# Optimization experiments

Measured on AMD Instinct MI355X. Metric: run time of the kernel, lower is better.

Reference implementation:

```python
import jax, jax.numpy as jnp
import numpy as np

SIZE = 128
WIN = SIZE // 4   # sliding-window size == region size (32)
HALF = WIN // 2   # 16


def _conv(x, w, pad, groups=1):
    return jax.lax.conv_general_dilated(x, w, (1, 1), [(pad, pad), (pad, pad)],
        dimension_numbers=('NCHW', 'OIHW', 'NCHW'), feature_group_count=groups)


def _resize(x, h, w):
    # F.interpolate(..., mode='bilinear', align_corners=False)
    return jax.image.resize(x, (x.shape[0], x.shape[1], h, w), 'bilinear', antialias=False)


def _gauss_kernels():
    ax = np.linspace(-2.0, 2.0, 5)
    xx, yy = np.meshgrid(ax, ax)
    g = np.exp(-(xx ** 2 + yy ** 2) / 2.0) / (2.0 * np.pi)  # sigma = 1
    gx = (-xx * g).astype(np.float32)
    gy = (-yy * g).astype(np.float32)
    return (jnp.asarray(np.tile(gx[None, None], (3, 3, 1, 1))),
            jnp.asarray(np.tile(gy[None, None], (3, 3, 1, 1))))


def _edge_extract(x):
    Gx, Gy = _gauss_kernels()
    h = _conv(x, Gx, 2)
    v = _conv(x, Gy, 2)
    return jnp.tanh(jnp.sqrt(h * h + v * v + 1e-8))


def _color_moments(x, win=5):
    # F.unfold-based local mean / unbiased var / skewness, via depthwise box sums
    C = x.shape[1]
    n = float(win * win)
    ones = jnp.ones((C, 1, win, win), x.dtype)
    box = lambda z: _conv(z, ones, win // 2, groups=C)
    s1 = box(x); s2 = box(x * x); s3 = box(x * x * x)
    mean = s1 / n
    var = (s2 - n * mean * mean) / (n - 1.0)               # unbiased, matches torch.var
    m3 = (s3 - 3.0 * mean * s2 + 2.0 * n * mean ** 3) / n  # E[(x-m)^3]
    skew = m3 / (jnp.sqrt(jnp.maximum(var, 0.0)) ** 3 + 1e-6)
    return jnp.concatenate([mean, var, skew], 1)


def _locate_region(c):
    # scipy: gradient magnitude < 0.2 -> 4-connected label at argmax -> bbox center
    H, W = c.shape
    flat = jnp.argmax(c)
    xm = (flat // W).astype(jnp.int32)
    ym = (flat % W).astype(jnp.int32)
    gm = jnp.hypot(jnp.gradient(c, axis=0), jnp.gradient(c, axis=1))
    mask = gm < 0.2
    seed = jnp.zeros((H, W), bool).at[xm, ym].set(True) & mask

    def dil(r):
        d = r
        d = d | jnp.pad(r[1:, :], ((0, 1), (0, 0)))
        d = d | jnp.pad(r[:-1, :], ((1, 0), (0, 0)))
        d = d | jnp.pad(r[:, 1:], ((0, 0), (0, 1)))
        d = d | jnp.pad(r[:, :-1], ((0, 0), (1, 0)))
        return d & mask

    def body(s):
        r, _ = s
        nr = dil(r)
        return (nr, jnp.any(nr != r))

    region, _ = jax.lax.while_loop(lambda s: s[1], body, (seed, jnp.any(seed)))
    rows = jnp.any(region, 1); cols = jnp.any(region, 0)
    rs = jnp.argmax(rows); re = H - jnp.argmax(rows[::-1])
    cs = jnp.argmax(cols); ce = W - jnp.argmax(cols[::-1])
    ok = mask[xm, ym]  # label_at_max != 0
    x1 = jnp.where(ok, ((rs + re) // 2).astype(jnp.int32), xm)
    y1 = jnp.where(ok, ((cs + ce) // 2).astype(jnp.int32), ym)
    return x1, y1


def _affine_grid(move, H, W):
    # theta = [[1,0,tx],[0,1,ty]] with (tx,ty)=move, align_corners=False
    bx = (2.0 * jnp.arange(W, dtype=jnp.float32) + 1.0) / W - 1.0
    by = (2.0 * jnp.arange(H, dtype=jnp.float32) + 1.0) / H - 1.0
    gx = bx[None, None, :] + move[:, 0, None, None]
    gy = by[None, :, None] + move[:, 1, None, None]
    return jnp.stack(jnp.broadcast_arrays(gx, gy), -1)  # [B,H,W,2]


def _grid_sample(x, grid):
    # bilinear, zeros padding, align_corners=False (torch defaults)
    B, C, H, W = x.shape
    ix = ((grid[..., 0] + 1.0) * W - 1.0) / 2.0
    iy = ((grid[..., 1] + 1.0) * H - 1.0) / 2.0
    ix0 = jnp.floor(ix).astype(jnp.int32)
    iy0 = jnp.floor(iy).astype(jnp.int32)
    wx1 = ix - ix0; wy1 = iy - iy0
    b = jnp.arange(B)[:, None, None]

    def g(yy, xx):
        valid = ((xx >= 0) & (xx < W) & (yy >= 0) & (yy < H)).astype(x.dtype)
        v = x[b, :, jnp.clip(yy, 0, H - 1), jnp.clip(xx, 0, W - 1)]  # [B,Hg,Wg,C]
        return v * valid[..., None]

    out = (g(iy0, ix0) * ((1 - wy1) * (1 - wx1))[..., None]
         + g(iy0, ix0 + 1) * ((1 - wy1) * wx1)[..., None]
         + g(iy0 + 1, ix0) * (wy1 * (1 - wx1))[..., None]
         + g(iy0 + 1, ix0 + 1) * (wy1 * wx1)[..., None])
    return jnp.transpose(out, (0, 3, 1, 2))


def _bn_relu6(x, w, b):
    # BatchNorm2d in training mode (batch stats, biased var, eps=1e-5) + ReLU6
    m = x.mean((0, 2, 3), keepdims=True)
    v = ((x - m) ** 2).mean((0, 2, 3), keepdims=True)
    y = (x - m) / jnp.sqrt(v + 1e-5) * w[None, :, None, None] + b[None, :, None, None]
    return jnp.clip(y, 0.0, 6.0)


def setup_inputs():
    key = jax.random.key(0)
    ks = jax.random.split(key, 8)
    B, C = 8, 64
    return dict(
        warm_flag=1,
        feat1=jax.random.normal(ks[0], (B, C, SIZE, SIZE), jnp.float32),
        feat2=jax.random.normal(ks[1], (B, C, SIZE, SIZE), jnp.float32),
        cam1=jax.random.uniform(ks[2], (B, 64, 64), jnp.float32),
        cam2=jax.random.uniform(ks[3], (B, 64, 64), jnp.float32),
        f_g=jax.random.uniform(ks[4], (B, 3, 512, 512), jnp.float32),
        f_e=jax.random.uniform(ks[5], (B, 3, 512, 512), jnp.float32),
        conv1_w=jax.random.normal(ks[6], (C, 3, 3, 3), jnp.float32) * 0.1,
        conv1_b=jnp.zeros((C,), jnp.float32),
        conv2_w=jax.random.normal(ks[7], (C, 9, 3, 3), jnp.float32) * 0.1,
        conv2_b=jnp.zeros((C,), jnp.float32),
        bn_w=jnp.ones((C,), jnp.float32),
        bn_b=jnp.zeros((C,), jnp.float32),
    )


def reference(warm_flag, feat1, feat2, cam1, cam2, f_g, f_e,
              conv1_w, conv1_b, conv2_w, conv2_b, bn_w, bn_b):
    B = cam1.shape[0]
    c1 = _resize(cam1[:, None], SIZE, SIZE)
    c2 = _resize(cam2[:, None], SIZE, SIZE)

    if warm_flag == 1:
        # numpy/scipy path in torch is detached from autograd
        c1s = jax.lax.stop_gradient(c1)
        c2s = jax.lax.stop_gradient(c2)
        x1, y1 = jax.vmap(_locate_region)(c1s[:, 0])
        # valid-mode box convolution of cam2 with ones((H//4, W//4)), argmax
        box = jax.lax.conv_general_dilated(c2s, jnp.ones((1, 1, WIN, WIN), c2.dtype), (1, 1),
            'VALID', dimension_numbers=('NCHW', 'OIHW', 'NCHW'))[:, 0]
        Wv = box.shape[-1]
        flat = jnp.argmax(box.reshape(B, -1), -1)
        x2 = (flat // Wv + HALF).astype(jnp.int32)
        y2 = (flat % Wv + HALF).astype(jnp.int32)

        idx = jnp.arange(SIZE)
        def rect(xc, yc):
            r = (idx[None, :] >= jnp.maximum(xc - HALF, 0)[:, None]) & \
                (idx[None, :] < jnp.minimum(xc + HALF, SIZE)[:, None])
            cc = (idx[None, :] >= jnp.maximum(yc - HALF, 0)[:, None]) & \
                 (idx[None, :] < jnp.minimum(yc + HALF, SIZE)[:, None])
            return r[:, None, :, None] & cc[:, None, None, :]
        mask1 = rect(x1, y1).astype(feat1.dtype)
        mask2 = rect(x2, y2).astype(feat2.dtype)
        mi1 = jnp.stack([x1, y1], -1).astype(jnp.float32)
        mi2 = jnp.stack([x2, y2], -1).astype(jnp.float32)
    else:
        mask1 = jnp.zeros_like(feat1)
        mask2 = jnp.zeros_like(feat2)
        mi1 = jnp.zeros((B, 2), jnp.float32)
        mi2 = jnp.zeros((B, 2), jnp.float32)

    cam2_move = (mi2 - mi1) / (SIZE // 2)
    cam1_move = (mi1 - mi2) / (SIZE // 2)
    grid1 = _affine_grid(cam1_move, SIZE, SIZE)
    grid2 = _affine_grid(cam2_move, SIZE, SIZE)

    moments = _resize(_color_moments(f_e), SIZE, SIZE)   # [B,9,128,128]
    edge = _resize(_edge_extract(f_g), SIZE, SIZE)       # [B,3,128,128]
    feat1_edge = jnp.clip(_conv(edge, conv1_w, 1) + conv1_b[None, :, None, None], 0.0, 6.0)
    feat2_color = _conv(moments, conv2_w, 1) + conv2_b[None, :, None, None]

    feat2_move = _grid_sample(feat2_color * mask2, grid2)
    feat1_edge_move = _grid_sample(feat1_edge * mask1, grid1)

    Bc, C, H, W = feat1.shape
    f1 = feat1.reshape(Bc, C, -1)
    f2 = feat2.reshape(Bc, C, -1)
    f2m = feat2_move.reshape(Bc, C, -1)
    f1m = feat1_edge_move.reshape(Bc, C, -1)

    f2_attn = jax.nn.softmax(jnp.einsum('bcn,bdn->bcd', f2m, f1), -1)  # [B,C,C]
    feat1_apply = jnp.einsum('bcd,bdn->bcn', f2_attn, f1).reshape(Bc, C, H, W)
    f1_attn = jax.nn.softmax(jnp.einsum('bcn,bdn->bcd', f1m, f2), -1)
    feat2_apply = jnp.einsum('bcd,bdn->bcn', f1_attn, f2).reshape(Bc, C, H, W)

    feat1_apply = _bn_relu6(feat1_apply, bn_w, bn_b)
    feat2_apply = _bn_relu6(feat2_apply, bn_w, bn_b)

    if warm_flag == 0:
        return (feat1, feat2, grid1, grid2, feat1_edge, feat2_color, f1_attn, f2_attn, feat1, feat2)
    return (feat1_apply, feat2_apply, grid1, grid2, feat1_edge, feat2_color, f1_attn, f2_attn, feat1, feat2)
```

## Files before the change

kernel.cpp:

```cpp
#include <hip/hip_runtime.h>
#include <math.h>

#define SIZE 128
#define WIN 32
#define HALF 16
#define B 8
#define C 64
#define N (SIZE*SIZE)
#define BCN 8388608
#define BV 97

#define O_APPLY1   0
#define O_APPLY2   8388608
#define O_GRID1    16777216
#define O_GRID2    17039360
#define O_EDGEF    17301504
#define O_COLORF   25690112
#define O_ATTN1    34078720
#define O_ATTN2    34111488
#define O_FEAT1    34144256
#define O_FEAT2    42532864

#define WS_C1      0
#define WS_C2      131072
#define WS_COLSUM  262144
#define WS_XY      361472
#define WS_MOM     361600
#define WS_EDGE    1541248
#define WS_LOG1    1672320
#define WS_LOG2    1705088
#define WS_BN      1737856

#define NEGINF (-3.402823466e+38f)

typedef unsigned __int128 u128;

__global__ void k_init(float* __restrict__ p, int n) {
  int i = blockIdx.x * 256 + threadIdx.x;
  if (i < n) p[i] = 0.f;
}

__global__ __launch_bounds__(256) void k_resize_cam(
    const float* __restrict__ cam1, const float* __restrict__ cam2,
    float* __restrict__ c1, float* __restrict__ c2) {
  int idx = blockIdx.x * 256 + threadIdx.x;
  int which = idx >> 17;
  int rem = idx & 131071;
  int b = rem >> 14, i = (rem >> 7) & 127, j = rem & 127;
  const float* s = (which ? cam2 : cam1) + b * 4096;
  float fy = fminf(fmaxf(0.5f * (float)i - 0.25f, 0.f), 63.f);
  float fx = fminf(fmaxf(0.5f * (float)j - 0.25f, 0.f), 63.f);
  int y0 = (int)fy; float ty = fy - (float)y0; int y1i = min(y0 + 1, 63);
  int x0 = (int)fx; float tx = fx - (float)x0; int x1i = min(x0 + 1, 63);
  float v00 = s[y0 * 64 + x0],  v01 = s[y0 * 64 + x1i];
  float v10 = s[y1i * 64 + x0], v11 = s[y1i * 64 + x1i];
  float v = (1.f - ty) * ((1.f - tx) * v00 + tx * v01)
          + ty * ((1.f - tx) * v10 + tx * v11);
  (which ? c2 : c1)[rem] = v;
}

__device__ __forceinline__ u128 hfill(u128 g, u128 m) {
  u128 p = m;
  g |= p & (g << 1);  p &= p << 1;
  g |= p & (g << 2);  p &= p << 2;
  g |= p & (g << 4);  p &= p << 4;
  g |= p & (g << 8);  p &= p << 8;
  g |= p & (g << 16); p &= p << 16;
  g |= p & (g << 32); p &= p << 32;
  g |= p & (g << 64);
  p = m;
  g |= p & (g >> 1);  p &= p >> 1;
  g |= p & (g >> 2);  p &= p >> 2;
  g |= p & (g >> 4);  p &= p >> 4;
  g |= p & (g >> 8);  p &= p >> 8;
  g |= p & (g >> 16); p &= p >> 16;
  g |= p & (g >> 32); p &= p >> 32;
  g |= p & (g >> 64);
  return g;
}

__global__ __launch_bounds__(256) void k_locate(const float* __restrict__ c1,
                                                int* __restrict__ xy) {
  int b = blockIdx.x;
  const float* c = c1 + b * N;
  int tid = threadIdx.x;
  __shared__ float sc[N];
  __shared__ float sv[256]; __shared__ int si[256];
  __shared__ unsigned int maskw[512];
  __shared__ unsigned long long glo[128], ghi[128];
  __shared__ unsigned long long rowany[2];
  __shared__ int s_changed, s_xm, s_ym, s_ok;

  float bv = NEGINF; int bi = 0;
  const float4* c4 = (const float4*)c;
  float4* sc4 = (float4*)sc;
  #pragma unroll
  for (int k = 0; k < 16; ++k) {
    int i4 = k * 256 + tid;
    float4 v = c4[i4];
    sc4[i4] = v;
    int base = i4 * 4;
    if (v.x > bv) { bv = v.x; bi = base; }
    if (v.y > bv) { bv = v.y; bi = base + 1; }
    if (v.z > bv) { bv = v.z; bi = base + 2; }
    if (v.w > bv) { bv = v.w; bi = base + 3; }
  }
  sv[tid] = bv; si[tid] = bi;
  __syncthreads();
  for (int s = 128; s; s >>= 1) {
    if (tid < s) {
      float ov = sv[tid + s]; int oi = si[tid + s];
      if (ov > sv[tid] || (ov == sv[tid] && oi < si[tid])) { sv[tid] = ov; si[tid] = oi; }
    }
    __syncthreads();
  }
  if (tid == 0) { s_xm = si[0] >> 7; s_ym = si[0] & 127; }

  #pragma unroll
  for (int q = 0; q < 2; ++q) {
    int w = tid + q * 256;
    int row = w >> 2, cb = (w & 3) * 32;
    unsigned int m = 0;
    for (int bit = 0; bit < 32; ++bit) {
      int i = row, j = cb + bit;
      float gx_, gy_;
      if (i == 0)        gx_ = sc[128 + j] - sc[j];
      else if (i == 127) gx_ = sc[127 * 128 + j] - sc[126 * 128 + j];
      else               gx_ = 0.5f * (sc[(i + 1) * 128 + j] - sc[(i - 1) * 128 + j]);
      if (j == 0)        gy_ = sc[i * 128 + 1] - sc[i * 128];
      else if (j == 127) gy_ = sc[i * 128 + 127] - sc[i * 128 + 126];
      else               gy_ = 0.5f * (sc[i * 128 + j + 1] - sc[i * 128 + j - 1]);
      if (hypotf(gx_, gy_) < 0.2f) m |= (1u << bit);
    }
    maskw[w] = m;
  }
  __syncthreads();
  if (tid == 0) {
    int w = (s_xm << 2) + (s_ym >> 5), bit = s_ym & 31;
    s_ok = (maskw[w] >> bit) & 1;
  }
  __syncthreads();

  int r = tid;
  u128 m = 0, g = 0;
  if (tid < 128) {
    m = ((u128)maskw[r * 4])
      | ((u128)maskw[r * 4 + 1] << 32)
      | ((u128)maskw[r * 4 + 2] << 64)
      | ((u128)maskw[r * 4 + 3] << 96);
    if (s_ok && r == s_xm) g = ((u128)1) << s_ym;
    g = hfill(g, m);
  }
  for (;;) {
    if (tid == 0) s_changed = 0;
    if (tid < 128) { glo[r] = (unsigned long long)g; ghi[r] = (unsigned long long)(g >> 64); }
    __syncthreads();
    if (tid < 128) {
      u128 gn = g;
      if (r > 0)   gn |= ((u128)glo[r - 1]) | ((u128)ghi[r - 1] << 64);
      if (r < 127) gn |= ((u128)glo[r + 1]) | ((u128)ghi[r + 1] << 64);
      gn &= m;
      gn = hfill(gn, m);
      if (gn != g) { g = gn; s_changed = 1; }
    }
    __syncthreads();
    if (!s_changed) break;
  }

  if (tid < 128) {
    unsigned long long ba = __ballot(g != 0);
    if ((tid & 63) == 0) rowany[tid >> 6] = ba;
    glo[r] = (unsigned long long)g; ghi[r] = (unsigned long long)(g >> 64);
  }
  __syncthreads();
  if (tid == 0) {
    unsigned long long r0 = rowany[0], r1 = rowany[1];
    unsigned long long cl = 0, ch = 0;
    for (int i = 0; i < 128; ++i) { cl |= glo[i]; ch |= ghi[i]; }
    int rs = 0, re = 0, cs = 0, ce = 0;
    if (r0 | r1) {
      rs = r0 ? (__ffsll(r0) - 1) : 64 + (__ffsll(r1) - 1);
      re = r1 ? 128 - __clzll(r1) : 64 - __clzll(r0);
      cs = cl ? (__ffsll(cl) - 1) : 64 + (__ffsll(ch) - 1);
      ce = ch ? 128 - __clzll(ch) : 64 - __clzll(cl);
    }
    int x1, y1;
    if (s_ok) { x1 = (rs + re) >> 1; y1 = (cs + ce) >> 1; }
    else      { x1 = s_xm;           y1 = s_ym; }
    xy[b] = x1; xy[8 + b] = y1;
  }
}

__global__ __launch_bounds__(256) void k_colsum(const float* __restrict__ c2,
                                                float* __restrict__ cs) {
  int idx = blockIdx.x * 256 + threadIdx.x;
  if (idx >= B * BV * 128) return;
  int cc = idx & 127, r = (idx >> 7) % BV, b = idx / (BV * 128);
  const float* s = c2 + b * N + cc;
  float acc = 0.f;
  #pragma unroll
  for (int dy = 0; dy < WIN; ++dy) acc += s[(r + dy) * 128];
  cs[idx] = acc;
}

__global__ __launch_bounds__(256) void k_boxargmax(const float* __restrict__ colsum,
                                                   int* __restrict__ xy) {
  int b = blockIdx.x, tid = threadIdx.x;
  const float* cs = colsum + b * BV * 128;
  float bv = NEGINF; int bi = 0;
  for (int p = tid; p < BV * BV; p += 256) {
    int r = p / BV, cc = p % BV;
    const float* row = cs + r * 128 + cc;
    float s = 0.f;
    #pragma unroll
    for (int dx = 0; dx < WIN; ++dx) s += row[dx];
    if (s > bv) { bv = s; bi = p; }
  }
  __shared__ float sv[256]; __shared__ int si[256];
  sv[tid] = bv; si[tid] = bi;
  __syncthreads();
  for (int s = 128; s; s >>= 1) {
    if (tid < s) {
      float ov = sv[tid + s]; int oi = si[tid + s];
      if (ov > sv[tid] || (ov == sv[tid] && oi < si[tid])) { sv[tid] = ov; si[tid] = oi; }
    }
    __syncthreads();
  }
  if (tid == 0) { xy[16 + b] = si[0] / BV + HALF; xy[24 + b] = si[0] % BV + HALF; }
}

__global__ __launch_bounds__(256) void k_grids(const int* __restrict__ xy,
                                               float* __restrict__ g1, float* __restrict__ g2) {
  int idx = blockIdx.x * 256 + threadIdx.x;
  int b = idx >> 14, h = (idx >> 7) & 127, w = idx & 127;
  float x1 = (float)xy[b], y1 = (float)xy[8 + b];
  float x2 = (float)xy[16 + b], y2 = (float)xy[24 + b];
  float bx = (2.f * (float)w + 1.f) / 128.f - 1.f;
  float by = (2.f * (float)h + 1.f) / 128.f - 1.f;
  float m1x = (x1 - x2) / 64.f, m1y = (y1 - y2) / 64.f;
  g1[idx * 2]     = bx + m1x; g1[idx * 2 + 1] = by + m1y;
  g2[idx * 2]     = bx - m1x; g2[idx * 2 + 1] = by - m1y;
}

__global__ __launch_bounds__(256) void k_moments(const float* __restrict__ fe,
                                                 float* __restrict__ mom) {
  int idx = blockIdx.x * 256 + threadIdx.x;
  int j = idx & 127, i = (idx >> 7) & 127, ch = (idx >> 14) % 3, b = idx / (3 * N);
  const float* src = fe + (size_t)(b * 3 + ch) * 262144;
  float s1a[6], s2a[6], s3a[6], s1b[6], s2b[6], s3b[6];
  #pragma unroll
  for (int t = 0; t < 6; ++t) {
    float a1 = 0, a2 = 0, a3 = 0, b1 = 0, b2 = 0, b3 = 0;
    int x = 4 * j - 1 + t;
    bool xo = (x >= 0 && x < 512);
    #pragma unroll
    for (int r = 0; r < 6; ++r) {
      int y = 4 * i - 1 + r;
      float v = (xo && y >= 0 && y < 512) ? src[y * 512 + x] : 0.f;
      float v2 = v * v, v3 = v2 * v;
      if (r < 5) { a1 += v; a2 += v2; a3 += v3; }
      if (r > 0) { b1 += v; b2 += v2; b3 += v3; }
    }
    s1a[t] = a1; s2a[t] = a2; s3a[t] = a3;
    s1b[t] = b1; s2b[t] = b2; s3b[t] = b3;
  }
  float am = 0, av = 0, as = 0;
  #pragma unroll
  for (int py = 0; py < 2; ++py) {
    #pragma unroll
    for (int px = 0; px < 2; ++px) {
      float s1 = 0, s2 = 0, s3 = 0;
      #pragma unroll
      for (int t = 0; t < 5; ++t) {
        s1 += py ? s1b[px + t] : s1a[px + t];
        s2 += py ? s2b[px + t] : s2a[px + t];
        s3 += py ? s3b[px + t] : s3a[px + t];
      }
      float mean = s1 / 25.f;
      float var  = (s2 - 25.f * mean * mean) / 24.f;
      float m3   = (s3 - 3.f * mean * s2 + 50.f * mean * mean * mean) / 25.f;
      float sq   = sqrtf(fmaxf(var, 0.f));
      float skew = m3 / (sq * sq * sq + 1e-6f);
      am += mean; av += var; as += skew;
    }
  }
  int base = (b * 9 + ch) * N + i * 128 + j;
  mom[base]         = 0.25f * am;
  mom[base + 3 * N] = 0.25f * av;
  mom[base + 6 * N] = 0.25f * as;
}

__global__ __launch_bounds__(256) void k_edge(const float* __restrict__ fg,
                                              float* __restrict__ edge) {
  int idx = blockIdx.x * 256 + threadIdx.x;
  int j = idx & 127, i = (idx >> 7) & 127, b = idx >> 14;
  const float* s0 = fg + (size_t)b * 3 * 262144;
  const float INV2PI = 0.15915494309189535f;
  float wg[5], ug[5];
  #pragma unroll
  for (int t = 0; t < 5; ++t) {
    float a = (float)t - 2.f;
    float e = expf(-0.5f * a * a);
    wg[t] = e; ug[t] = -a * e;
  }
  float rAa[6], rAb[6], rBa[6], rBb[6];
  #pragma unroll
  for (int t = 0; t < 6; ++t) {
    float aa = 0, ab = 0, ba = 0, bb = 0;
    int x = 4 * j - 1 + t;
    bool xo = (x >= 0 && x < 512);
    #pragma unroll
    for (int r = 0; r < 6; ++r) {
      int y = 4 * i - 1 + r;
      float v = 0.f;
      if (xo && y >= 0 && y < 512) {
        int o = y * 512 + x;
        v = s0[o] + s0[262144 + o] + s0[524288 + o];
      }
      if (r < 5) { aa += v * wg[r]; ba += v * ug[r]; }
      if (r > 0) { ab += v * wg[r - 1]; bb += v * ug[r - 1]; }
    }
    rAa[t] = aa; rAb[t] = ab; rBa[t] = ba; rBb[t] = bb;
  }
  float acc = 0.f;
  #pragma unroll
  for (int py = 0; py < 2; ++py) {
    #pragma unroll
    for (int px = 0; px < 2; ++px) {
      float h = 0, v = 0;
      #pragma unroll
      for (int t = 0; t < 5; ++t) {
        float A  = py ? rAb[px + t] : rAa[px + t];
        float Bw = py ? rBb[px + t] : rBa[px + t];
        h += A * ug[t];
        v += Bw * wg[t];
      }
      h *= INV2PI; v *= INV2PI;
      acc += tanhf(sqrtf(h * h + v * v + 1e-8f));
    }
  }
  edge[idx] = 0.25f * acc;
}

__global__ __launch_bounds__(256) void k_conv1(const float* __restrict__ edge,
                                               const float* __restrict__ w,
                                               const float* __restrict__ bias,
                                               float* __restrict__ out) {
  int b = blockIdx.x >> 6, tile = blockIdx.x & 63;
  int ti0 = (tile >> 3) * 16, tj0 = (tile & 7) * 16;
  __shared__ float et[18 * 18];
  __shared__ float ws1[64 * 12];
  int tid = threadIdx.x;
  for (int l = tid; l < 324; l += 256) {
    int r = l / 18, cc = l % 18;
    int gi = ti0 + r - 1, gj = tj0 + cc - 1;
    et[l] = (gi >= 0 && gi < 128 && gj >= 0 && gj < 128) ? edge[b * N + gi * 128 + gj] : 0.f;
  }
  for (int l = tid; l < 64 * 12; l += 256) {
    int o = l / 12, t = l % 12;
    ws1[l] = (t < 9) ? (w[o * 27 + t] + w[o * 27 + 9 + t] + w[o * 27 + 18 + t]) : 0.f;
  }
  __syncthreads();
  int i = tid >> 4, j = tid & 15;
  float win[12];
  #pragma unroll
  for (int dy = 0; dy < 3; ++dy)
    #pragma unroll
    for (int dx = 0; dx < 3; ++dx)
      win[dy * 3 + dx] = et[(i + dy) * 18 + (j + dx)];
  win[9] = 0.f; win[10] = 0.f; win[11] = 0.f;
  float* o = out + (size_t)b * C * N + (ti0 + i) * 128 + tj0 + j;
  for (int oc = 0; oc < C; ++oc) {
    const float4* wr = (const float4*)(ws1 + oc * 12);
    float acc = bias[oc];
    #pragma unroll
    for (int q = 0; q < 3; ++q) {
      float4 w4 = wr[q];
      acc += w4.x * win[4 * q] + w4.y * win[4 * q + 1]
           + w4.z * win[4 * q + 2] + w4.w * win[4 * q + 3];
    }
    o[oc * N] = fminf(fmaxf(acc, 0.f), 6.f);
  }
}

__global__ __launch_bounds__(256) void k_conv2(const float* __restrict__ mom,
                                               const float* __restrict__ w,
                                               const float* __restrict__ bias,
                                               float* __restrict__ out) {
  int b = blockIdx.x >> 6, tile = blockIdx.x & 63;
  int ti0 = (tile >> 3) * 16, tj0 = (tile & 7) * 16;
  __shared__ float mt[9 * 324];
  __shared__ float w2s[64 * 84];
  int tid = threadIdx.x;
  for (int l = tid; l < 9 * 324; l += 256) {
    int ic = l / 324, rem = l % 324, r = rem / 18, cc = rem % 18;
    int gi = ti0 + r - 1, gj = tj0 + cc - 1;
    mt[l] = (gi >= 0 && gi < 128 && gj >= 0 && gj < 128) ? mom[(b * 9 + ic) * N + gi * 128 + gj] : 0.f;
  }
  for (int l = tid; l < 64 * 84; l += 256) {
    int o = l / 84, t = l % 84;
    w2s[l] = (t < 81) ? w[o * 81 + t] : 0.f;
  }
  __syncthreads();
  int i = tid >> 4, j = tid & 15;
  float win[84];
  #pragma unroll
  for (int ic = 0; ic < 9; ++ic)
    #pragma unroll
    for (int dy = 0; dy < 3; ++dy)
      #pragma unroll
      for (int dx = 0; dx < 3; ++dx)
        win[ic * 9 + dy * 3 + dx] = mt[ic * 324 + (i + dy) * 18 + (j + dx)];
  win[81] = 0.f; win[82] = 0.f; win[83] = 0.f;
  float* o = out + (size_t)b * C * N + (ti0 + i) * 128 + tj0 + j;
  for (int oc = 0; oc < C; ++oc) {
    const float4* wr = (const float4*)(w2s + oc * 84);
    float acc = bias[oc];
    #pragma unroll
    for (int q = 0; q < 21; ++q) {
      float4 w4 = wr[q];
      acc += w4.x * win[4 * q] + w4.y * win[4 * q + 1]
           + w4.z * win[4 * q + 2] + w4.w * win[4 * q + 3];
    }
    o[oc * N] = acc;
  }
}

__global__ __launch_bounds__(256) void k_logits(const float* __restrict__ aBase,
                                                const float* __restrict__ bBase,
                                                float* __restrict__ out,
                                                const int* __restrict__ xy, int mode) {
  int b = blockIdx.x >> 4, sl = blockIdx.x & 15;
  int x1 = xy[b], y1 = xy[8 + b], x2 = xy[16 + b], y2 = xy[24 + b];
  int dyh, dxw, rlo, rhi, clo, chi;
  if (mode == 0) {
    dyh = y1 - y2; dxw = x1 - x2;
    rlo = max(x1 - HALF, 0); rhi = min(x1 + HALF, SIZE);
    clo = max(y1 - HALF, 0); chi = min(y1 + HALF, SIZE);
  } else {
    dyh = y2 - y1; dxw = x2 - x1;
    rlo = max(x2 - HALF, 0); rhi = min(x2 + HALF, SIZE);
    clo = max(y2 - HALF, 0); chi = min(y2 + HALF, SIZE);
  }
  int hlo = max(0, rlo - dyh), hhi = min(SIZE, rhi - dyh);
  int wlo = max(0, clo - dxw), whi = min(SIZE, chi - dxw);
  int wn = whi - wlo, hn = hhi - hlo;
  int npos = (wn > 0 && hn > 0) ? wn * hn : 0;
  if (sl * 64 >= npos) return;

  __shared__ float aS[64][65];
  __shared__ float bS[64][65];
  int tid = threadIdx.x;
  const float* aB = aBase + (size_t)b * C * N;
  const float* bB = bBase + (size_t)b * C * N;
  for (int l = tid; l < 4096; l += 256) {
    int ch = l >> 6, k = l & 63;
    int p = sl * 64 + k;
    float av = 0.f, bv = 0.f;
    if (p < npos) {
      int h = hlo + p / wn, w = wlo + p % wn;
      av = aB[ch * N + (h + dyh) * 128 + (w + dxw)];
      bv = bB[ch * N + h * 128 + w];
    }
    aS[ch][k] = av; bS[ch][k] = bv;
  }
  __syncthreads();
  int ci = (tid >> 4) << 2, di = (tid & 15) << 2;
  float acc[4][4] = {};
  #pragma unroll 4
  for (int k = 0; k < 64; ++k) {
    float a0 = aS[ci][k], a1 = aS[ci + 1][k], a2 = aS[ci + 2][k], a3 = aS[ci + 3][k];
    float b0 = bS[di][k], b1 = bS[di + 1][k], b2 = bS[di + 2][k], b3 = bS[di + 3][k];
    acc[0][0] += a0 * b0; acc[0][1] += a0 * b1; acc[0][2] += a0 * b2; acc[0][3] += a0 * b3;
    acc[1][0] += a1 * b0; acc[1][1] += a1 * b1; acc[1][2] += a1 * b2; acc[1][3] += a1 * b3;
    acc[2][0] += a2 * b0; acc[2][1] += a2 * b1; acc[2][2] += a2 * b2; acc[2][3] += a2 * b3;
    acc[3][0] += a3 * b0; acc[3][1] += a3 * b1; acc[3][2] += a3 * b2; acc[3][3] += a3 * b3;
  }
  float* o = out + b * 4096;
  #pragma unroll
  for (int u = 0; u < 4; ++u)
    #pragma unroll
    for (int v = 0; v < 4; ++v)
      atomicAdd(&o[(ci + u) * 64 + (di + v)], acc[u][v]);
}

__global__ void k_softmax(const float* __restrict__ l1, const float* __restrict__ l2,
                          float* __restrict__ o6, float* __restrict__ o7) {
  int row = blockIdx.x;
  const float* src = blockIdx.y ? l2 : l1;
  float* dst = blockIdx.y ? o7 : o6;
  int lane = threadIdx.x;
  float v = src[row * 64 + lane];
  float mx = v;
  for (int off = 32; off; off >>= 1) mx = fmaxf(mx, __shfl_xor(mx, off));
  float e = expf(v - mx);
  float s = e;
  for (int off = 32; off; off >>= 1) s += __shfl_xor(s, off);
  dst[row * 64 + lane] = e / s;
}

__global__ __launch_bounds__(256) void k_apply(const float* __restrict__ a1,
                                               const float* __restrict__ s1_,
                                               float* __restrict__ d1,
                                               const float* __restrict__ a2,
                                               const float* __restrict__ s2_,
                                               float* __restrict__ d2) {
  const float* attn; const float* src; float* dst;
  if (blockIdx.y == 0) { attn = a1; src = s1_; dst = d1; }
  else                 { attn = a2; src = s2_; dst = d2; }
  int b = blockIdx.x >> 6, chunk = blockIdx.x & 63;
  int n0 = chunk * 256 + threadIdx.x;
  __shared__ __align__(16) float at[4096];
  for (int l = threadIdx.x; l < 4096; l += 256) at[l] = attn[b * 4096 + l];
  __syncthreads();
  const float* s = src + (size_t)b * C * N + n0;
  float v[64];
  #pragma unroll
  for (int d = 0; d < 64; ++d) v[d] = s[d * N];
  float* o = dst + (size_t)b * C * N + n0;
  for (int c = 0; c < 64; ++c) {
    const float4* ar = (const float4*)(at + c * 64);
    float acc = 0.f;
    #pragma unroll
    for (int q = 0; q < 16; ++q) {
      float4 w4 = ar[q];
      acc += w4.x * v[4 * q] + w4.y * v[4 * q + 1] + w4.z * v[4 * q + 2] + w4.w * v[4 * q + 3];
    }
    o[c * N] = acc;
  }
}

__global__ __launch_bounds__(256) void k_bnstats1(const float* __restrict__ t0,
                                                  const float* __restrict__ t1,
                                                  float* __restrict__ part) {
  int c = blockIdx.x, b = blockIdx.y, t = blockIdx.z;
  const float* src = (t ? t1 : t0) + (size_t)(b * C + c) * N;
  const float4* s4 = (const float4*)src;
  float s = 0.f, ss = 0.f;
  #pragma unroll
  for (int k = 0; k < 16; ++k) {
    float4 v = s4[k * 256 + threadIdx.x];
    s  += v.x + v.y + v.z + v.w;
    ss += v.x * v.x + v.y * v.y + v.z * v.z + v.w * v.w;
  }
  for (int off = 32; off; off >>= 1) {
    s  += __shfl_xor(s, off);
    ss += __shfl_xor(ss, off);
  }
  __shared__ float as[4], ass[4];
  int wave = threadIdx.x >> 6;
  if ((threadIdx.x & 63) == 0) { as[wave] = s; ass[wave] = ss; }
  __syncthreads();
  if (threadIdx.x == 0) {
    int idx = (t * C + c) * B + b;
    part[idx]        = as[0] + as[1] + as[2] + as[3];
    part[1024 + idx] = ass[0] + ass[1] + ass[2] + ass[3];
  }
}

__global__ void k_bnstats2(const float* __restrict__ part, float* __restrict__ stats) {
  int i = threadIdx.x;
  int t = i >> 6, c = i & 63;
  float s = 0.f, ss = 0.f;
  #pragma unroll
  for (int b = 0; b < B; ++b) {
    int idx = (t * C + c) * B + b;
    s  += part[idx];
    ss += part[1024 + idx];
  }
  float mean = s / 131072.f;
  float var  = ss / 131072.f - mean * mean;
  stats[t * 128 + c]      = mean;
  stats[t * 128 + 64 + c] = 1.f / sqrtf(var + 1e-5f);
}

__global__ __launch_bounds__(256) void k_bnapply(float* __restrict__ t0, float* __restrict__ t1,
                                                 const float* __restrict__ stats,
                                                 const float* __restrict__ bw,
                                                 const float* __restrict__ bb) {
  int e = blockIdx.x * 256 + threadIdx.x;
  int t = blockIdx.y;
  float* p = t ? t1 : t0;
  int c = (e >> 14) & 63;
  float m = stats[t * 128 + c], r = stats[t * 128 + 64 + c];
  float y = (p[e] - m) * r * bw[c] + bb[c];
  p[e] = fminf(fmaxf(y, 0.f), 6.f);
}

__global__ __launch_bounds__(256) void k_copy2(const float4* __restrict__ s1, float4* __restrict__ d1,
                                               const float4* __restrict__ s2, float4* __restrict__ d2) {
  int i = blockIdx.x * 256 + threadIdx.x;
  d1[i] = s1[i];
  d2[i] = s2[i];
}

extern "C" void kernel_launch(void* const* d_in, const int* in_sizes, int n_in,
                              void* d_out, int out_size, void* d_ws, size_t ws_size,
                              hipStream_t stream) {
  const float* feat1   = (const float*)d_in[1];
  const float* feat2   = (const float*)d_in[2];
  const float* cam1    = (const float*)d_in[3];
  const float* cam2    = (const float*)d_in[4];
  const float* f_g     = (const float*)d_in[5];
  const float* f_e     = (const float*)d_in[6];
  const float* conv1_w = (const float*)d_in[7];
  const float* conv1_b = (const float*)d_in[8];
  const float* conv2_w = (const float*)d_in[9];
  const float* conv2_b = (const float*)d_in[10];
  const float* bn_w    = (const float*)d_in[11];
  const float* bn_b    = (const float*)d_in[12];

  float* out = (float*)d_out;
  float* w = (float*)d_ws;
  int* xy = (int*)(w + WS_XY);

  float* o0 = out + O_APPLY1;
  float* o1 = out + O_APPLY2;
  float* o2 = out + O_GRID1;
  float* o3 = out + O_GRID2;
  float* o4 = out + O_EDGEF;
  float* o5 = out + O_COLORF;
  float* o6 = out + O_ATTN1;
  float* o7 = out + O_ATTN2;
  float* o8 = out + O_FEAT1;
  float* o9 = out + O_FEAT2;

  k_init<<<(65536 + 255) / 256, 256, 0, stream>>>(w + WS_LOG1, 65536);

  k_resize_cam<<<1024, 256, 0, stream>>>(cam1, cam2, w + WS_C1, w + WS_C2);
  k_locate<<<B, 256, 0, stream>>>(w + WS_C1, xy);
  k_colsum<<<(B * BV * 128 + 255) / 256, 256, 0, stream>>>(w + WS_C2, w + WS_COLSUM);
  k_boxargmax<<<B, 256, 0, stream>>>(w + WS_COLSUM, xy);
  k_grids<<<B * N / 256, 256, 0, stream>>>(xy, o2, o3);

  k_moments<<<B * 3 * N / 256, 256, 0, stream>>>(f_e, w + WS_MOM);
  k_edge<<<B * N / 256, 256, 0, stream>>>(f_g, w + WS_EDGE);
  k_conv1<<<B * 64, 256, 0, stream>>>(w + WS_EDGE, conv1_w, conv1_b, o4);
  k_conv2<<<B * 64, 256, 0, stream>>>(w + WS_MOM, conv2_w, conv2_b, o5);

  k_copy2<<<BCN / 4 / 256, 256, 0, stream>>>((const float4*)feat1, (float4*)o8,
                                             (const float4*)feat2, (float4*)o9);

  k_logits<<<B * 16, 256, 0, stream>>>(o4, feat2, w + WS_LOG1, xy, 0);
  k_logits<<<B * 16, 256, 0, stream>>>(o5, feat1, w + WS_LOG2, xy, 1);

  k_softmax<<<dim3(B * C, 2), 64, 0, stream>>>(w + WS_LOG1, w + WS_LOG2, o6, o7);

  k_apply<<<dim3(B * 64, 2), 256, 0, stream>>>(o7, feat1, o0, o6, feat2, o1);

  k_bnstats1<<<dim3(C, B, 2), 256, 0, stream>>>(o0, o1, w + WS_LOG1);
  k_bnstats2<<<1, 128, 0, stream>>>(w + WS_LOG1, w + WS_BN);

  k_bnapply<<<dim3(BCN / 256, 2), 256, 0, stream>>>(o0, o1, w + WS_BN, bn_w, bn_b);
}
```

Baseline: 635.7 us.

## Tile moments and edge kernels through shared memory, merge logits launches

The moments and edge kernels now stage a 66x66 input halo tile in shared memory per 16x16 output tile, so the overlapping 6x6 stencil windows are not re-read from global memory for every thread. The two logits launches are merged into one launch using blockIdx.y to pick the mode. The apply kernel drops its shared-memory staging of the attention matrix and reads it through the cache as float4 instead. The trade-off is more shared-memory use and bank-access patterns in the stencil kernels, and in the apply kernel the attention matrix is now read from global/cache rather than from LDS.

Measured after the change: 640.6 us. No clear change (+0.8%).

```diff
diff --git a/kernel.cpp b/kernel.cpp
--- a/kernel.cpp
+++ b/kernel.cpp
@@ -244,19 +244,29 @@
 
 __global__ __launch_bounds__(256) void k_moments(const float* __restrict__ fe,
                                                  float* __restrict__ mom) {
-  int idx = blockIdx.x * 256 + threadIdx.x;
-  int j = idx & 127, i = (idx >> 7) & 127, ch = (idx >> 14) % 3, b = idx / (3 * N);
+  int blk = blockIdx.x;
+  int tile = blk & 63, ch = (blk >> 6) % 3, b = blk / 192;
+  int ti0 = (tile >> 3) * 16, tj0 = (tile & 7) * 16;
   const float* src = fe + (size_t)(b * 3 + ch) * 262144;
+  __shared__ float sx[66 * 66];
+  int oy0 = 4 * ti0 - 1, ox0 = 4 * tj0 - 1;
+  int tid = threadIdx.x;
+  for (int l = tid; l < 66 * 66; l += 256) {
+    int r = l / 66, cc = l % 66;
+    int gy = oy0 + r, gx = ox0 + cc;
+    sx[l] = (gy >= 0 && gy < 512 && gx >= 0 && gx < 512) ? src[gy * 512 + gx] : 0.f;
+  }
+  __syncthreads();
+  int ii = tid >> 4, jj = tid & 15;
+  int i = ti0 + ii, j = tj0 + jj;
   float s1a[6], s2a[6], s3a[6], s1b[6], s2b[6], s3b[6];
   #pragma unroll
   for (int t = 0; t < 6; ++t) {
     float a1 = 0, a2 = 0, a3 = 0, b1 = 0, b2 = 0, b3 = 0;
-    int x = 4 * j - 1 + t;
-    bool xo = (x >= 0 && x < 512);
+    int lx = 4 * jj + t;
     #pragma unroll
     for (int r = 0; r < 6; ++r) {
-      int y = 4 * i - 1 + r;
-      float v = (xo && y >= 0 && y < 512) ? src[y * 512 + x] : 0.f;
+      float v = sx[(4 * ii + r) * 66 + lx];
       float v2 = v * v, v3 = v2 * v;
       if (r < 5) { a1 += v; a2 += v2; a3 += v3; }
       if (r > 0) { b1 += v; b2 += v2; b3 += v3; }
@@ -292,9 +302,26 @@
 
 __global__ __launch_bounds__(256) void k_edge(const float* __restrict__ fg,
                                               float* __restrict__ edge) {
-  int idx = blockIdx.x * 256 + threadIdx.x;
-  int j = idx & 127, i = (idx >> 7) & 127, b = idx >> 14;
+  int blk = blockIdx.x;
+  int tile = blk & 63, b = blk >> 6;
+  int ti0 = (tile >> 3) * 16, tj0 = (tile & 7) * 16;
   const float* s0 = fg + (size_t)b * 3 * 262144;
+  __shared__ float sx[66 * 66];
+  int oy0 = 4 * ti0 - 1, ox0 = 4 * tj0 - 1;
+  int tid = threadIdx.x;
+  for (int l = tid; l < 66 * 66; l += 256) {
+    int r = l / 66, cc = l % 66;
+    int gy = oy0 + r, gx = ox0 + cc;
+    float v = 0.f;
+    if (gy >= 0 && gy < 512 && gx >= 0 && gx < 512) {
+      int o = gy * 512 + gx;
+      v = s0[o] + s0[262144 + o] + s0[524288 + o];
+    }
+    sx[l] = v;
+  }
+  __syncthreads();
+  int ii = tid >> 4, jj = tid & 15;
+  int i = ti0 + ii, j = tj0 + jj;
   const float INV2PI = 0.15915494309189535f;
   float wg[5], ug[5];
   #pragma unroll
@@ -307,16 +334,10 @@
   #pragma unroll
   for (int t = 0; t < 6; ++t) {
     float aa = 0, ab = 0, ba = 0, bb = 0;
-    int x = 4 * j - 1 + t;
-    bool xo = (x >= 0 && x < 512);
+    int lx = 4 * jj + t;
     #pragma unroll
     for (int r = 0; r < 6; ++r) {
-      int y = 4 * i - 1 + r;
-      float v = 0.f;
-      if (xo && y >= 0 && y < 512) {
-        int o = y * 512 + x;
-        v = s0[o] + s0[262144 + o] + s0[524288 + o];
-      }
+      float v = sx[(4 * ii + r) * 66 + lx];
       if (r < 5) { aa += v * wg[r]; ba += v * ug[r]; }
       if (r > 0) { ab += v * wg[r - 1]; bb += v * ug[r - 1]; }
     }
@@ -339,7 +360,7 @@
       acc += tanhf(sqrtf(h * h + v * v + 1e-8f));
     }
   }
-  edge[idx] = 0.25f * acc;
+  edge[b * N + i * 128 + j] = 0.25f * acc;
 }
 
 __global__ __launch_bounds__(256) void k_conv1(const float* __restrict__ edge,
@@ -426,10 +447,17 @@
   }
 }
 
-__global__ __launch_bounds__(256) void k_logits(const float* __restrict__ aBase,
-                                                const float* __restrict__ bBase,
-                                                float* __restrict__ out,
-                                                const int* __restrict__ xy, int mode) {
+__global__ __launch_bounds__(256) void k_logits(const float* __restrict__ aB1,
+                                                const float* __restrict__ bB1,
+                                                float* __restrict__ out1,
+                                                const float* __restrict__ aB2,
+                                                const float* __restrict__ bB2,
+                                                float* __restrict__ out2,
+                                                const int* __restrict__ xy) {
+  int mode = blockIdx.y;
+  const float* aBase = mode ? aB2 : aB1;
+  const float* bBase = mode ? bB2 : bB1;
+  float* out = mode ? out2 : out1;
   int b = blockIdx.x >> 4, sl = blockIdx.x & 15;
   int x1 = xy[b], y1 = xy[8 + b], x2 = xy[16 + b], y2 = xy[24 + b];
   int dyh, dxw, rlo, rhi, clo, chi;
@@ -510,20 +538,17 @@
   else                 { attn = a2; src = s2_; dst = d2; }
   int b = blockIdx.x >> 6, chunk = blockIdx.x & 63;
   int n0 = chunk * 256 + threadIdx.x;
-  __shared__ __align__(16) float at[4096];
-  for (int l = threadIdx.x; l < 4096; l += 256) at[l] = attn[b * 4096 + l];
-  __syncthreads();
   const float* s = src + (size_t)b * C * N + n0;
   float v[64];
   #pragma unroll
   for (int d = 0; d < 64; ++d) v[d] = s[d * N];
+  const float4* at4 = (const float4*)(attn + b * 4096);
   float* o = dst + (size_t)b * C * N + n0;
   for (int c = 0; c < 64; ++c) {
-    const float4* ar = (const float4*)(at + c * 64);
     float acc = 0.f;
     #pragma unroll
     for (int q = 0; q < 16; ++q) {
-      float4 w4 = ar[q];
+      float4 w4 = at4[c * 16 + q];
       acc += w4.x * v[4 * q] + w4.y * v[4 * q + 1] + w4.z * v[4 * q + 2] + w4.w * v[4 * q + 3];
     }
     o[c * N] = acc;
@@ -633,16 +658,16 @@
   k_boxargmax<<<B, 256, 0, stream>>>(w + WS_COLSUM, xy);
   k_grids<<<B * N / 256, 256, 0, stream>>>(xy, o2, o3);
 
-  k_moments<<<B * 3 * N / 256, 256, 0, stream>>>(f_e, w + WS_MOM);
-  k_edge<<<B * N / 256, 256, 0, stream>>>(f_g, w + WS_EDGE);
+  k_moments<<<B * 3 * 64, 256, 0, stream>>>(f_e, w + WS_MOM);
+  k_edge<<<B * 64, 256, 0, stream>>>(f_g, w + WS_EDGE);
   k_conv1<<<B * 64, 256, 0, stream>>>(w + WS_EDGE, conv1_w, conv1_b, o4);
   k_conv2<<<B * 64, 256, 0, stream>>>(w + WS_MOM, conv2_w, conv2_b, o5);
 
   k_copy2<<<BCN / 4 / 256, 256, 0, stream>>>((const float4*)feat1, (float4*)o8,
                                              (const float4*)feat2, (float4*)o9);
 
-  k_logits<<<B * 16, 256, 0, stream>>>(o4, feat2, w + WS_LOG1, xy, 0);
-  k_logits<<<B * 16, 256, 0, stream>>>(o5, feat1, w + WS_LOG2, xy, 1);
+  k_logits<<<dim3(B * 16, 2), 256, 0, stream>>>(o4, feat2, w + WS_LOG1,
+                                                o5, feat1, w + WS_LOG2, xy);
 
   k_softmax<<<dim3(B * C, 2), 64, 0, stream>>>(w + WS_LOG1, w + WS_LOG2, o6, o7);
 
```
